# Optimization experiments

Measured on AMD Instinct MI355X. Metric: run time of the kernel, lower is better.

## Reference

```python
import jax, jax.numpy as jnp
import numpy as np


def setup_inputs() -> dict:
    key = jax.random.key(0)
    ks = jax.random.split(key, 6)
    B, T, D, H = 32, 2048, 1024, 1024
    s = jax.random.normal(ks[0], (1, B, D), dtype=jnp.float32)
    h = jax.random.normal(ks[1], (B, T, D), dtype=jnp.float32)
    mask = jax.random.randint(ks[2], (B, T), 0, 2, dtype=jnp.int32)
    W = jax.random.normal(ks[3], (D, H), dtype=jnp.float32) * (6.0 / (D + H)) ** 0.5
    U = jax.random.normal(ks[4], (D, H), dtype=jnp.float32) * (6.0 / (D + H)) ** 0.5
    v = jax.random.normal(ks[5], (H, 1), dtype=jnp.float32) * (6.0 / (H + 1)) ** 0.5
    return {"s": s, "h": h, "mask": mask, "W": W, "U": U, "v": v}


def reference(s, h, mask, W, U, v):
    # mask-fill encoder states: zero out padded timesteps
    m = (mask != 0)[:, :, None]            # (B, T, 1)
    h = jnp.where(m, h, 0.0)               # (B, T, D)
    s_t = jnp.transpose(s, (1, 0, 2))      # (B, 1, D)
    proj_s = s_t @ W                       # (B, 1, H)
    proj_h = h @ U                         # (B, T, H)
    energy = jnp.tanh(proj_s + proj_h) @ v  # (B, T, 1)
    energy = jnp.where(m, energy, -1e9)
    score = jax.nn.softmax(energy, axis=1)  # softmax over time
    context = jnp.sum(score * h, axis=1)    # (B, D)
    return context
```

## Files before the change

kernel.cpp:

```cpp
#include <hip/hip_runtime.h>
#include <hip/hip_fp16.h>
#include <math.h>

#define BB 32
#define TT 2048
#define DD 1024
#define HH 1024
#define MM (BB*TT)

typedef _Float16 half8 __attribute__((ext_vector_type(8)));
typedef float f32x4 __attribute__((ext_vector_type(4)));

__device__ __forceinline__ float tanh_fast(float x) {
    float cx = fminf(fmaxf(x, -10.0f), 10.0f);
    float e2 = __expf(2.0f * cx);
    return (e2 - 1.0f) / (e2 + 1.0f);
}

__device__ __forceinline__ void load_lds16(const _Float16* g, _Float16* l) {
    __builtin_amdgcn_global_load_lds(
        (const __attribute__((address_space(1))) void*)g,
        (__attribute__((address_space(3))) void*)l, 16, 0, 0);
}

#define CAST_BLOCKS (MM/2)
#define UT_BLOCKS   1024
#define PS_BLOCKS   128
#define CPT_BLOCKS  32
#define TOTAL_SETUP (CAST_BLOCKS + UT_BLOCKS + PS_BLOCKS + CPT_BLOCKS)

__global__ __launch_bounds__(256)
void mega_setup_kernel(const float* __restrict__ h,
                       const int* __restrict__ mask,
                       _Float16* __restrict__ h16,
                       const float* __restrict__ U,
                       _Float16* __restrict__ Ut,
                       const float* __restrict__ s,
                       const float* __restrict__ W,
                       float* __restrict__ ps,
                       float* __restrict__ out,
                       int* __restrict__ rowlist,
                       int* __restrict__ cnts) {
    __shared__ float smem[1056];
    __shared__ int wsum[4];
    const int bid = blockIdx.x;
    const int tid = threadIdx.x;

    if (bid < CAST_BLOCKS) {
        const int row = bid * 2 + (tid >> 7);
        if (mask[row] == 0) return;
        const int c = (tid & 127) * 8;
        const long base = (long)row * DD + c;
        const float4 f0 = *(const float4*)(h + base);
        const float4 f1 = *(const float4*)(h + base + 4);
        half8 o;
        o[0] = (_Float16)f0.x; o[1] = (_Float16)f0.y;
        o[2] = (_Float16)f0.z; o[3] = (_Float16)f0.w;
        o[4] = (_Float16)f1.x; o[5] = (_Float16)f1.y;
        o[6] = (_Float16)f1.z; o[7] = (_Float16)f1.w;
        *(half8*)(h16 + base) = o;
        return;
    }

    if (bid < CAST_BLOCKS + UT_BLOCKS) {
        const int id = bid - CAST_BLOCKS;
        const int bx = id & 31, by = id >> 5;
        float (*tile)[33] = (float(*)[33])smem;
        const int tx = tid & 31, ty = tid >> 5;
#pragma unroll
        for (int j = 0; j < 4; ++j)
            tile[ty + j * 8][tx] = U[(long)(by * 32 + ty + j * 8) * HH + bx * 32 + tx];
        __syncthreads();
#pragma unroll
        for (int j = 0; j < 4; ++j)
            Ut[(long)(bx * 32 + ty + j * 8) * DD + by * 32 + tx] =
                (_Float16)tile[tx][ty + j * 8];
        return;
    }

    if (bid < CAST_BLOCKS + UT_BLOCKS + PS_BLOCKS) {
        const int id = bid - (CAST_BLOCKS + UT_BLOCKS);
        const int b = id & 31, nseg = id >> 5;
        const int n = nseg * 256 + tid;
        float* ss = smem;
#pragma unroll
        for (int j = 0; j < 4; ++j)
            ss[tid + j * 256] = s[b * DD + tid + j * 256];
        out[b * DD + n] = 0.0f;
        __syncthreads();
        float a[8];
#pragma unroll
        for (int j = 0; j < 8; ++j) a[j] = 0.f;
        for (int d = 0; d < DD; d += 8) {
#pragma unroll
            for (int j = 0; j < 8; ++j)
                a[j] += ss[d + j] * W[(long)(d + j) * HH + n];
        }
        ps[b * HH + n] = ((a[0]+a[1])+(a[2]+a[3])) + ((a[4]+a[5])+(a[6]+a[7]));
        return;
    }

    {
        const int b = bid - (CAST_BLOCKS + UT_BLOCKS + PS_BLOCKS);
        const int lane = tid & 63, w = tid >> 6;
        const int* mb = mask + b * TT;
        const int t0 = tid * 8;
        int m[8], c = 0;
#pragma unroll
        for (int j = 0; j < 8; ++j) { m[j] = (mb[t0 + j] != 0); c += m[j]; }
        int pref = c;
#pragma unroll
        for (int off = 1; off < 64; off <<= 1) {
            int nv = __shfl_up(pref, off, 64);
            if (lane >= off) pref += nv;
        }
        if (lane == 63) wsum[w] = pref;
        __syncthreads();
        int wbase = 0;
        for (int i = 0; i < w; ++i) wbase += wsum[i];
        int pos = wbase + pref - c;
#pragma unroll
        for (int j = 0; j < 8; ++j)
            if (m[j]) rowlist[b * TT + pos++] = t0 + j;
        const int total = wsum[0] + wsum[1] + wsum[2] + wsum[3];
        if (tid == 0) cnts[b] = total;
        __syncthreads();
        const int padded = ((total + 127) >> 7) << 7;
        const int lastt = (total > 0) ? rowlist[b * TT + total - 1] : 0;
        for (int ci = total + tid; ci < padded; ci += 256)
            rowlist[b * TT + ci] = lastt;
    }
}

#define Bb_K 32

__global__ __launch_bounds__(256)
void energy_gemm_kernel(const _Float16* __restrict__ h16,
                        const _Float16* __restrict__ Ut,
                        const float* __restrict__ ps,
                        const float* __restrict__ v,
                        const int* __restrict__ rowlist,
                        const int* __restrict__ cnts,
                        float* __restrict__ epart) {
    const int mt = blockIdx.x;
    const int nt = blockIdx.y;
    const int b   = mt >> 4;
    const int ci0 = (mt & 15) << 7;
    if (ci0 >= cnts[b]) return;

    __shared__ _Float16 As[128][32];
    __shared__ _Float16 Bs[128][32];
    __shared__ float ps_s[128];
    __shared__ float v_s[128];
    __shared__ int   rl[128];

    const int n0  = nt * 128;
    const int tid = threadIdx.x;
    const int wave = tid >> 6, lane = tid & 63;
    const int wm = wave >> 1, wn = wave & 1;

    if (tid < 128) {
        ps_s[tid] = ps[b * HH + n0 + tid];
        v_s[tid]  = v[n0 + tid];
        rl[tid]   = rowlist[b * TT + ci0 + tid];
    }
    __syncthreads();

    const int srow = wave * 32 + (lane >> 2);
    const int sseg = ((lane & 3) ^ ((lane >> 2) & 3)) * 8;
    const _Float16* gA0 = h16 + ((long)b * TT + rl[srow])      * DD + sseg;
    const _Float16* gA1 = h16 + ((long)b * TT + rl[srow + 16]) * DD + sseg;
    const _Float16* gB0 = Ut + (long)(n0 + srow) * DD + sseg;
    const _Float16* gB1 = gB0 + 16 * DD;
    _Float16* lA0 = &As[wave * 32][0];
    _Float16* lA1 = &As[wave * 32 + 16][0];
    _Float16* lB0 = &Bs[wave * 32][0];
    _Float16* lB1 = &Bs[wave * 32 + 16][0];

    f32x4 acc[4][4];
#pragma unroll
    for (int i = 0; i < 4; ++i)
#pragma unroll
        for (int j = 0; j < 4; ++j) acc[i][j] = (f32x4)0.0f;

    const int lr = lane & 15;
    const int lk = (((lane >> 4) ^ (lr & 3))) * 8;

#pragma unroll 1
    for (int k0 = 0; k0 < DD; k0 += Bb_K) {
        __syncthreads();
        load_lds16(gA0 + k0, lA0);
        load_lds16(gA1 + k0, lA1);
        load_lds16(gB0 + k0, lB0);
        load_lds16(gB1 + k0, lB1);
        __syncthreads();

        half8 af[4], bf[4];
#pragma unroll
        for (int tm = 0; tm < 4; ++tm)
            af[tm] = *(const half8*)&As[wm * 64 + tm * 16 + lr][lk];
#pragma unroll
        for (int tn = 0; tn < 4; ++tn)
            bf[tn] = *(const half8*)&Bs[wn * 64 + tn * 16 + lr][lk];
        __builtin_amdgcn_s_setprio(1);
#pragma unroll
        for (int tm = 0; tm < 4; ++tm)
#pragma unroll
            for (int tn = 0; tn < 4; ++tn)
                acc[tm][tn] = __builtin_amdgcn_mfma_f32_16x16x32_f16(
                    af[tm], bf[tn], acc[tm][tn], 0, 0, 0);
        __builtin_amdgcn_s_setprio(0);
    }

    float part[4][4];
#pragma unroll
    for (int tm = 0; tm < 4; ++tm) {
#pragma unroll
        for (int r = 0; r < 4; ++r) {
            float p = 0.f;
#pragma unroll
            for (int tn = 0; tn < 4; ++tn) {
                const int cl = wn * 64 + tn * 16 + lr;
                p += v_s[cl] * tanh_fast(acc[tm][tn][r] + ps_s[cl]);
            }
            part[tm][r] = p;
        }
    }
#pragma unroll
    for (int off = 1; off < 16; off <<= 1)
#pragma unroll
        for (int tm = 0; tm < 4; ++tm)
#pragma unroll
            for (int r = 0; r < 4; ++r)
                part[tm][r] += __shfl_xor(part[tm][r], off, 64);

    if ((lane & 15) == 0) {
        const int slot = nt * 2 + wn;
#pragma unroll
        for (int tm = 0; tm < 4; ++tm)
#pragma unroll
            for (int r = 0; r < 4; ++r) {
                const int ci = ci0 + wm * 64 + tm * 16 + (lane >> 4) * 4 + r;
                epart[(long)slot * MM + b * TT + ci] = part[tm][r];
            }
    }
}

__global__ void softmax_kernel(const float* __restrict__ epart,
                               const int* __restrict__ rowlist,
                               const int* __restrict__ cnts,
                               float* __restrict__ score) {
    const int b = blockIdx.x, tid = threadIdx.x;
    const int cnt = cnts[b];
    for (int t = tid; t < TT; t += 256) score[b * TT + t] = 0.0f;

    float e[8], mx = -1e30f;
#pragma unroll
    for (int i = 0; i < 8; ++i) {
        const int ci = i * 256 + tid;
        float sum = -1e30f;
        if (ci < cnt) {
            sum = 0.f;
#pragma unroll
            for (int p = 0; p < 16; ++p)
                sum += epart[(long)p * MM + b * TT + ci];
        }
        e[i] = sum;
        mx = fmaxf(mx, sum);
    }
#pragma unroll
    for (int off = 32; off > 0; off >>= 1) mx = fmaxf(mx, __shfl_xor(mx, off, 64));
    __shared__ float r4[4];
    if ((tid & 63) == 0) r4[tid >> 6] = mx;
    __syncthreads();
    mx = fmaxf(fmaxf(r4[0], r4[1]), fmaxf(r4[2], r4[3]));

    float tot = 0.f;
#pragma unroll
    for (int i = 0; i < 8; ++i) {
        const int ci = i * 256 + tid;
        e[i] = (ci < cnt) ? __expf(e[i] - mx) : 0.0f;
        tot += e[i];
    }
#pragma unroll
    for (int off = 32; off > 0; off >>= 1) tot += __shfl_xor(tot, off, 64);
    __shared__ float s4[4];
    if ((tid & 63) == 0) s4[tid >> 6] = tot;
    __syncthreads();
    tot = s4[0] + s4[1] + s4[2] + s4[3];
    const float inv = 1.0f / tot;
#pragma unroll
    for (int i = 0; i < 8; ++i) {
        const int ci = i * 256 + tid;
        if (ci < cnt)
            score[b * TT + rowlist[b * TT + ci]] = e[i] * inv;
    }
}

__global__ void context_kernel(const _Float16* __restrict__ h16,
                               const float* __restrict__ score,
                               float* __restrict__ out) {
    const int tc = blockIdx.x;
    const int b  = blockIdx.y;
    const int d0 = threadIdx.x * 8;
    float a[8];
#pragma unroll
    for (int j = 0; j < 8; ++j) a[j] = 0.f;
    for (int i = 0; i < 128; ++i) {
        const int t = tc * 128 + i;
        const float sc = score[(long)b * TT + t];
        if (sc != 0.0f) {
            const half8 hv = *(const half8*)(h16 + ((long)(b * TT + t)) * DD + d0);
#pragma unroll
            for (int j = 0; j < 8; ++j) a[j] += sc * (float)hv[j];
        }
    }
#pragma unroll
    for (int j = 0; j < 8; ++j) atomicAdd(&out[b * DD + d0 + j], a[j]);
}

extern "C" void kernel_launch(void* const* d_in, const int* in_sizes, int n_in,
                              void* d_out, int out_size, void* d_ws, size_t ws_size,
                              hipStream_t stream) {
    const float* s    = (const float*)d_in[0];
    const float* h    = (const float*)d_in[1];
    const int*   mask = (const int*)  d_in[2];
    const float* W    = (const float*)d_in[3];
    const float* U    = (const float*)d_in[4];
    const float* v    = (const float*)d_in[5];
    float* out = (float*)d_out;

    char* ws = (char*)d_ws;
    size_t off = 0;
    _Float16* h16 = (_Float16*)(ws + off); off += (size_t)MM * DD * 2;
    _Float16* Ut  = (_Float16*)(ws + off); off += (size_t)HH * DD * 2;
    float*    ps  = (float*)(ws + off);    off += (size_t)BB * HH * 4;
    float*    ep  = (float*)(ws + off);    off += (size_t)16 * MM * 4;
    float*    scr = (float*)(ws + off);    off += (size_t)MM * 4;
    int*      rlist = (int*)(ws + off);    off += (size_t)MM * 4;
    int*      cnts  = (int*)(ws + off);    off += 64 * 4;

    mega_setup_kernel<<<TOTAL_SETUP, 256, 0, stream>>>(h, mask, h16, U, Ut,
                                                       s, W, ps, out, rlist, cnts);
    energy_gemm_kernel<<<dim3(512, 8), 256, 0, stream>>>(h16, Ut, ps, v,
                                                         rlist, cnts, ep);
    softmax_kernel<<<BB, 256, 0, stream>>>(ep, rlist, cnts, scr);
    context_kernel<<<dim3(16, 32), 128, 0, stream>>>(h16, scr, out);
}
```

Before: 616.8 us.

## Double-buffer LDS tiles in energy GEMM and swap grid order for A-tile reuse

Energy GEMM now double-buffers the A and B LDS tiles so the global-to-LDS load of the next K slice overlaps the MFMAs on the current one, needing one barrier per step instead of two. The grid is transposed so the eight N tiles sharing an M tile launch together, which should improve L2 reuse of the gathered h rows. The XOR swizzle on LDS is removed, which may bring back bank conflicts on the fragment reads, and the setprio hints are dropped. LDS use doubles.

```diff
diff --git a/kernel.cpp b/kernel.cpp
--- a/kernel.cpp
+++ b/kernel.cpp
@@ -142,14 +142,14 @@
                         const int* __restrict__ rowlist,
                         const int* __restrict__ cnts,
                         float* __restrict__ epart) {
-    const int mt = blockIdx.x;
-    const int nt = blockIdx.y;
+    const int nt = blockIdx.x;
+    const int mt = blockIdx.y;
     const int b   = mt >> 4;
     const int ci0 = (mt & 15) << 7;
     if (ci0 >= cnts[b]) return;
 
-    __shared__ _Float16 As[128][32];
-    __shared__ _Float16 Bs[128][32];
+    __shared__ _Float16 As[2][128][32];
+    __shared__ _Float16 Bs[2][128][32];
     __shared__ float ps_s[128];
     __shared__ float v_s[128];
     __shared__ int   rl[128];
@@ -167,15 +167,11 @@
     __syncthreads();
 
     const int srow = wave * 32 + (lane >> 2);
-    const int sseg = ((lane & 3) ^ ((lane >> 2) & 3)) * 8;
+    const int sseg = (lane & 3) * 8;
     const _Float16* gA0 = h16 + ((long)b * TT + rl[srow])      * DD + sseg;
     const _Float16* gA1 = h16 + ((long)b * TT + rl[srow + 16]) * DD + sseg;
     const _Float16* gB0 = Ut + (long)(n0 + srow) * DD + sseg;
     const _Float16* gB1 = gB0 + 16 * DD;
-    _Float16* lA0 = &As[wave * 32][0];
-    _Float16* lA1 = &As[wave * 32 + 16][0];
-    _Float16* lB0 = &Bs[wave * 32][0];
-    _Float16* lB1 = &Bs[wave * 32 + 16][0];
 
     f32x4 acc[4][4];
 #pragma unroll
@@ -183,34 +179,48 @@
 #pragma unroll
         for (int j = 0; j < 4; ++j) acc[i][j] = (f32x4)0.0f;
 
+    const int lk = (lane >> 4) * 8;
     const int lr = lane & 15;
-    const int lk = (((lane >> 4) ^ (lr & 3))) * 8;
+
+    load_lds16(gA0, &As[0][wave * 32][0]);
+    load_lds16(gA1, &As[0][wave * 32 + 16][0]);
+    load_lds16(gB0, &Bs[0][wave * 32][0]);
+    load_lds16(gB1, &Bs[0][wave * 32 + 16][0]);
+    asm volatile("s_waitcnt vmcnt(0)" ::: "memory");
+    __builtin_amdgcn_s_barrier();
+
+#define KSTEP(CUR, NXT, KS)                                                   \
+    {                                                                         \
+        const int k1 = ((KS) + 1) * Bb_K;                                     \
+        if (k1 < DD) {                                                        \
+            load_lds16(gA0 + k1, &As[NXT][wave * 32][0]);                     \
+            load_lds16(gA1 + k1, &As[NXT][wave * 32 + 16][0]);                \
+            load_lds16(gB0 + k1, &Bs[NXT][wave * 32][0]);                     \
+            load_lds16(gB1 + k1, &Bs[NXT][wave * 32 + 16][0]);                \
+        }                                                                     \
+        half8 af[4], bf[4];                                                   \
+        _Pragma("unroll")                                                     \
+        for (int tm = 0; tm < 4; ++tm)                                        \
+            af[tm] = *(const half8*)&As[CUR][wm * 64 + tm * 16 + lr][lk];     \
+        _Pragma("unroll")                                                     \
+        for (int tn = 0; tn < 4; ++tn)                                        \
+            bf[tn] = *(const half8*)&Bs[CUR][wn * 64 + tn * 16 + lr][lk];     \
+        _Pragma("unroll")                                                     \
+        for (int tm = 0; tm < 4; ++tm)                                        \
+            _Pragma("unroll")                                                 \
+            for (int tn = 0; tn < 4; ++tn)                                    \
+                acc[tm][tn] = __builtin_amdgcn_mfma_f32_16x16x32_f16(         \
+                    af[tm], bf[tn], acc[tm][tn], 0, 0, 0);                    \
+        asm volatile("s_waitcnt vmcnt(0)" ::: "memory");                      \
+        __builtin_amdgcn_s_barrier();                                         \
+    }
 
 #pragma unroll 1
-    for (int k0 = 0; k0 < DD; k0 += Bb_K) {
-        __syncthreads();
-        load_lds16(gA0 + k0, lA0);
-        load_lds16(gA1 + k0, lA1);
-        load_lds16(gB0 + k0, lB0);
-        load_lds16(gB1 + k0, lB1);
-        __syncthreads();
-
-        half8 af[4], bf[4];
-#pragma unroll
-        for (int tm = 0; tm < 4; ++tm)
-            af[tm] = *(const half8*)&As[wm * 64 + tm * 16 + lr][lk];
-#pragma unroll
-        for (int tn = 0; tn < 4; ++tn)
-            bf[tn] = *(const half8*)&Bs[wn * 64 + tn * 16 + lr][lk];
-        __builtin_amdgcn_s_setprio(1);
-#pragma unroll
-        for (int tm = 0; tm < 4; ++tm)
-#pragma unroll
-            for (int tn = 0; tn < 4; ++tn)
-                acc[tm][tn] = __builtin_amdgcn_mfma_f32_16x16x32_f16(
-                    af[tm], bf[tn], acc[tm][tn], 0, 0, 0);
-        __builtin_amdgcn_s_setprio(0);
-    }
+    for (int ks = 0; ks < 32; ks += 2) {
+        KSTEP(0, 1, ks);
+        KSTEP(1, 0, ks + 1);
+    }
+#undef KSTEP
 
     float part[4][4];
 #pragma unroll
@@ -342,7 +352,7 @@
 
     mega_setup_kernel<<<TOTAL_SETUP, 256, 0, stream>>>(h, mask, h16, U, Ut,
                                                        s, W, ps, out, rlist, cnts);
-    energy_gemm_kernel<<<dim3(512, 8), 256, 0, stream>>>(h16, Ut, ps, v,
+    energy_gemm_kernel<<<dim3(8, 512), 256, 0, stream>>>(h16, Ut, ps, v,
                                                          rlist, cnts, ep);
     softmax_kernel<<<BB, 256, 0, stream>>>(ep, rlist, cnts, scr);
     context_kernel<<<dim3(16, 32), 128, 0, stream>>>(h16, scr, out);
```

Result: faster. 562.1 us (-8.9%).

## Enlarge energy GEMM tile to 128x256 with K=64 and 8 waves

Applied to the files above, without the earlier changes.

The energy GEMM block tile grows from 128x128 to 128x256 with 512 threads (8 waves in a 2x4 layout), and the K step doubles to 64 with two MFMA sub-steps per barrier pair. The grid is reordered so the N tiles of one M tile run in adjacent blocks, sharing the gathered A rows in cache. The goal is fewer barriers per unit of work and more reuse of each loaded tile. In exchange the LDS XOR swizzle is dropped, so the 128-byte LDS rows may cause bank conflicts on fragment reads. Larger blocks also reduce how many blocks fit on each CU.

```diff
diff --git a/kernel.cpp b/kernel.cpp
--- a/kernel.cpp
+++ b/kernel.cpp
@@ -132,9 +132,9 @@
     }
 }
 
-#define Bb_K 32
-
-__global__ __launch_bounds__(256)
+#define Bb_K 64
+
+__global__ __launch_bounds__(512)
 void energy_gemm_kernel(const _Float16* __restrict__ h16,
                         const _Float16* __restrict__ Ut,
                         const float* __restrict__ ps,
@@ -142,74 +142,77 @@
                         const int* __restrict__ rowlist,
                         const int* __restrict__ cnts,
                         float* __restrict__ epart) {
-    const int mt = blockIdx.x;
-    const int nt = blockIdx.y;
+    const int nt = blockIdx.x;
+    const int mt = blockIdx.y;
     const int b   = mt >> 4;
     const int ci0 = (mt & 15) << 7;
     if (ci0 >= cnts[b]) return;
 
-    __shared__ _Float16 As[128][32];
-    __shared__ _Float16 Bs[128][32];
-    __shared__ float ps_s[128];
-    __shared__ float v_s[128];
+    __shared__ _Float16 As[128][64];
+    __shared__ _Float16 Bs[256][64];
+    __shared__ float ps_s[256];
+    __shared__ float v_s[256];
     __shared__ int   rl[128];
 
-    const int n0  = nt * 128;
+    const int n0  = nt * 256;
     const int tid = threadIdx.x;
     const int wave = tid >> 6, lane = tid & 63;
-    const int wm = wave >> 1, wn = wave & 1;
-
-    if (tid < 128) {
+    const int wm = wave >> 2, wn = wave & 3;
+
+    if (tid < 256) {
         ps_s[tid] = ps[b * HH + n0 + tid];
         v_s[tid]  = v[n0 + tid];
-        rl[tid]   = rowlist[b * TT + ci0 + tid];
-    }
+    }
+    if (tid < 128) rl[tid] = rowlist[b * TT + ci0 + tid];
     __syncthreads();
 
-    const int srow = wave * 32 + (lane >> 2);
-    const int sseg = ((lane & 3) ^ ((lane >> 2) & 3)) * 8;
-    const _Float16* gA0 = h16 + ((long)b * TT + rl[srow])      * DD + sseg;
-    const _Float16* gA1 = h16 + ((long)b * TT + rl[srow + 16]) * DD + sseg;
-    const _Float16* gB0 = Ut + (long)(n0 + srow) * DD + sseg;
-    const _Float16* gB1 = gB0 + 16 * DD;
-    _Float16* lA0 = &As[wave * 32][0];
-    _Float16* lA1 = &As[wave * 32 + 16][0];
-    _Float16* lB0 = &Bs[wave * 32][0];
-    _Float16* lB1 = &Bs[wave * 32 + 16][0];
+    const int sr  = lane >> 3;
+    const int sseg = (lane & 7) * 8;
+    const int ra0 = wave * 16 + sr;
+    const int ra1 = wave * 16 + 8 + sr;
+    const _Float16* gA0 = h16 + ((long)b * TT + rl[ra0]) * DD + sseg;
+    const _Float16* gA1 = h16 + ((long)b * TT + rl[ra1]) * DD + sseg;
+    const _Float16* gB0 = Ut + (long)(n0 + wave * 32 + sr)      * DD + sseg;
+    const _Float16* gB1 = gB0 + 8  * DD;
+    const _Float16* gB2 = gB0 + 16 * DD;
+    const _Float16* gB3 = gB0 + 24 * DD;
 
     f32x4 acc[4][4];
 #pragma unroll
     for (int i = 0; i < 4; ++i)
 #pragma unroll
-        for (int j = 0; j < 4; ++j) acc[i][j] = (f32x4)0.0f;
-
+        for (int j2 = 0; j2 < 4; ++j2) acc[i][j2] = (f32x4)0.0f;
+
+    const int lk = (lane >> 4) * 8;
     const int lr = lane & 15;
-    const int lk = (((lane >> 4) ^ (lr & 3))) * 8;
 
 #pragma unroll 1
     for (int k0 = 0; k0 < DD; k0 += Bb_K) {
         __syncthreads();
-        load_lds16(gA0 + k0, lA0);
-        load_lds16(gA1 + k0, lA1);
-        load_lds16(gB0 + k0, lB0);
-        load_lds16(gB1 + k0, lB1);
-        __syncthreads();
-
-        half8 af[4], bf[4];
-#pragma unroll
-        for (int tm = 0; tm < 4; ++tm)
-            af[tm] = *(const half8*)&As[wm * 64 + tm * 16 + lr][lk];
-#pragma unroll
-        for (int tn = 0; tn < 4; ++tn)
-            bf[tn] = *(const half8*)&Bs[wn * 64 + tn * 16 + lr][lk];
-        __builtin_amdgcn_s_setprio(1);
-#pragma unroll
-        for (int tm = 0; tm < 4; ++tm)
+        load_lds16(gA0 + k0, &As[wave * 16][0]);
+        load_lds16(gA1 + k0, &As[wave * 16 + 8][0]);
+        load_lds16(gB0 + k0, &Bs[wave * 32][0]);
+        load_lds16(gB1 + k0, &Bs[wave * 32 + 8][0]);
+        load_lds16(gB2 + k0, &Bs[wave * 32 + 16][0]);
+        load_lds16(gB3 + k0, &Bs[wave * 32 + 24][0]);
+        __syncthreads();
+
+#pragma unroll
+        for (int ks = 0; ks < 2; ++ks) {
+            half8 af[4], bf[4];
+#pragma unroll
+            for (int tm = 0; tm < 4; ++tm)
+                af[tm] = *(const half8*)&As[wm * 64 + tm * 16 + lr][ks * 32 + lk];
 #pragma unroll
             for (int tn = 0; tn < 4; ++tn)
-                acc[tm][tn] = __builtin_amdgcn_mfma_f32_16x16x32_f16(
-                    af[tm], bf[tn], acc[tm][tn], 0, 0, 0);
-        __builtin_amdgcn_s_setprio(0);
+                bf[tn] = *(const half8*)&Bs[wn * 64 + tn * 16 + lr][ks * 32 + lk];
+#pragma unroll
+            for (int tm = 0; tm < 4; ++tm)
+#pragma unroll
+                for (int tn = 0; tn < 4; ++tn)
+                    acc[tm][tn] = __builtin_amdgcn_mfma_f32_16x16x32_f16(
+                        af[tm], bf[tn], acc[tm][tn], 0, 0, 0);
+        }
     }
 
     float part[4][4];
@@ -235,7 +238,7 @@
                 part[tm][r] += __shfl_xor(part[tm][r], off, 64);
 
     if ((lane & 15) == 0) {
-        const int slot = nt * 2 + wn;
+        const int slot = nt * 4 + wn;
 #pragma unroll
         for (int tm = 0; tm < 4; ++tm)
 #pragma unroll
@@ -342,7 +345,7 @@
 
     mega_setup_kernel<<<TOTAL_SETUP, 256, 0, stream>>>(h, mask, h16, U, Ut,
                                                        s, W, ps, out, rlist, cnts);
-    energy_gemm_kernel<<<dim3(512, 8), 256, 0, stream>>>(h16, Ut, ps, v,
+    energy_gemm_kernel<<<dim3(4, 512), 512, 0, stream>>>(h16, Ut, ps, v,
                                                          rlist, cnts, ep);
     softmax_kernel<<<BB, 256, 0, stream>>>(ep, rlist, cnts, scr);
     context_kernel<<<dim3(16, 32), 128, 0, stream>>>(h16, scr, out);
```

New measurement: 584.6 us. 1.06x faster.
